# Optimization experiments

Measured on AMD Instinct MI355X. Metric: run time of the kernel, lower is better.

## Reference

```python
import jax, jax.numpy as jnp
import numpy as np

IN_CAPS = 1152
OUT_CAPS = 10
IN_DIM = 8
OUT_DIM = 16
ROUTING_ITERS = 3
BATCH = 512


def squash(s, axis=-1, eps=1e-8):
    # v = (||s||^2 / (1 + ||s||^2)) * s / ||s||
    mag_sq = jnp.sum(s * s, axis=axis, keepdims=True)
    mag = jnp.sqrt(mag_sq + eps)
    return (mag_sq / (1.0 + mag_sq)) * (s / mag)


def setup_inputs() -> dict:
    key = jax.random.key(0)
    kx, kw = jax.random.split(key)
    x = jax.random.normal(kx, (BATCH, IN_CAPS, IN_DIM), dtype=jnp.float32)
    stdv = 1.0 / np.sqrt(IN_CAPS)
    W = jax.random.uniform(kw, (IN_CAPS, OUT_CAPS, OUT_DIM, IN_DIM),
                           minval=-stdv, maxval=stdv, dtype=jnp.float32)
    return {"x": x, "W": W}


def reference(x, W):
    # u_hat[b,i,j,:] = W[i,j] @ x[b,i]  -> [B, 1152, 10, 16]
    u_hat = jnp.einsum('ijde,bie->bijd', W, x)
    u_det = jax.lax.stop_gradient(u_hat)
    b = jnp.zeros((x.shape[0], IN_CAPS, OUT_CAPS), dtype=x.dtype)
    v = None
    for it in range(ROUTING_ITERS):
        c = jax.nn.softmax(b, axis=2)  # softmax over out capsules
        u = u_hat if it == ROUTING_ITERS - 1 else u_det
        s = jnp.einsum('bij,bijd->bjd', c, u)  # [B, 10, 16]
        v = squash(s, axis=-1)
        if it != ROUTING_ITERS - 1:
            # agreement: u_hat . v  -> [B, 1152, 10]
            b = b + jnp.einsum('bijd,bjd->bij', u_det, v)
    return v  # [B, 10, 16]
```

## Files before the change

### kernel.cpp

```cpp
#include <hip/hip_runtime.h>
#include <math.h>

#define J 10
#define BT 16
#define NBT 32
#define NIC 16
#define ICB 72
#define IPW 18
#define JD 160
#define BATCH 512
#define IN_CAPS 1152
#define RTH 256

typedef __attribute__((ext_vector_type(8))) short short8;
typedef __attribute__((ext_vector_type(4))) float f32x4;

__device__ inline short f2bf(float f) {
    union { float f; unsigned u; } v; v.f = f;
    return (short)((v.u + 0x7FFFu + ((v.u >> 16) & 1u)) >> 16);
}
__device__ inline short8 cvt8(float4 a, float4 b) {
    short8 o;
    o[0] = f2bf(a.x); o[1] = f2bf(a.y); o[2] = f2bf(a.z); o[3] = f2bf(a.w);
    o[4] = f2bf(b.x); o[5] = f2bf(b.y); o[6] = f2bf(b.z); o[7] = f2bf(b.w);
    return o;
}

__global__ __launch_bounds__(256) void convert_w(
    const float* __restrict__ W, short* __restrict__ Wb, short* __restrict__ zb)
{
    const int t = blockIdx.x * 256 + threadIdx.x;
    const float4* src = (const float4*)W + (size_t)t * 2;
    *(short8*)(Wb + (size_t)t * 8) = cvt8(src[0], src[1]);
    if (blockIdx.x == 0 && threadIdx.x < 32) zb[threadIdx.x] = 0;
}

#define TI 32
#define TB 64
__global__ __launch_bounds__(256) void transpose_x(
    const float* __restrict__ X, short* __restrict__ Xb)
{
    __shared__ short8 tile[TI][TB + 1];
    const int it = blockIdx.x % (IN_CAPS / TI);
    const int bt = blockIdx.x / (IN_CAPS / TI);
    const int t  = threadIdx.x;

    const int i_l = t & 31, b_s = t >> 5;
#pragma unroll
    for (int p = 0; p < 8; ++p) {
        const int b_l = p * 8 + b_s;
        const float4* src = (const float4*)(X +
            (((size_t)(bt * TB + b_l)) * IN_CAPS + it * TI + i_l) * 8);
        tile[i_l][b_l] = cvt8(src[0], src[1]);
    }
    __syncthreads();
    const int b_l = t & 63, i_s = t >> 6;
#pragma unroll
    for (int p = 0; p < 8; ++p) {
        const int i_l2 = p * 4 + i_s;
        *(short8*)(Xb + (((size_t)(it * TI + i_l2)) * BATCH + bt * TB + b_l) * 8)
            = tile[i_l2][b_l];
    }
}

template<int MODE>
__global__ __launch_bounds__(RTH, 2) void route_kernel(
    const short* __restrict__ Xb, const short* __restrict__ Wb,
    const short* __restrict__ zb, const float* __restrict__ V,
    float* __restrict__ S_part)
{
    __shared__ float s_lds[BT][JD + 1];
    const int tid   = threadIdx.x;
    const int lane  = tid & 63, wave = tid >> 6;
    const int icb   = blockIdx.x % NIC;
    const int btile = blockIdx.x / NIC;
    const int bcol  = lane & 15, kg = lane >> 4;
    const int b     = btile * BT + bcol;

    for (int t = tid; t < BT * (JD + 1); t += RTH) (&s_lds[0][0])[t] = 0.f;
    __syncthreads();

    if (MODE == 0) {
        f32x4 acc[J];
#pragma unroll
        for (int j = 0; j < J; ++j) acc[j] = (f32x4)(0.f);
        for (int ks = wave; ks < ICB / 4; ks += 4) {
            const int ia = icb * ICB + ks * 4 + kg;
            const short8 bfr = *(const short8*)(Xb + ((size_t)ia * BATCH + b) * 8);
            short8 afr[J];
#pragma unroll
            for (int j = 0; j < J; ++j)
                afr[j] = *(const short8*)(Wb + (size_t)ia * 1280 + j * 128 + bcol * 8);
#pragma unroll
            for (int j = 0; j < J; ++j)
                acc[j] = __builtin_amdgcn_mfma_f32_16x16x32_bf16(afr[j], bfr, acc[j], 0, 0, 0);
        }
#pragma unroll
        for (int j = 0; j < J; ++j)
#pragma unroll
            for (int r = 0; r < 4; ++r)
                atomicAdd(&s_lds[bcol][j * 16 + kg * 4 + r], 0.1f * acc[j][r]);
    } else {
        float4 Vr[J];
#pragma unroll
        for (int j = 0; j < J; ++j)
            Vr[j] = *(const float4*)(V + (size_t)b * JD + j * 16 + kg * 4);

        float s_acc[J][4];
#pragma unroll
        for (int j = 0; j < J; ++j)
#pragma unroll
            for (int r = 0; r < 4; ++r) s_acc[j][r] = 0.f;

        const bool act = (lane < 16);
        const short* xb0 = act ? (Xb + (size_t)b * 8) : zb;
        const size_t xis = act ? (size_t)BATCH * 8 : 0;
        const short* wb0 = act ? (Wb + (size_t)bcol * 8) : zb;
        const size_t wis = act ? 1280 : 0;
        const int    wjs = act ? 128 : 0;

        const int i0w = icb * ICB + wave * IPW;
        for (int ii = 0; ii < IPW; ++ii) {
            const size_t i = (size_t)(i0w + ii);
            short8 afr[J];
#pragma unroll
            for (int j = 0; j < J; ++j)
                afr[j] = *(const short8*)(wb0 + i * wis + j * wjs);
            const short8 bfr = *(const short8*)(xb0 + i * xis);

            f32x4 u[J];
#pragma unroll
            for (int j = 0; j < J; ++j)
                u[j] = __builtin_amdgcn_mfma_f32_16x16x32_bf16(afr[j], bfr, (f32x4)(0.f), 0, 0, 0);

            float L[J];
#pragma unroll
            for (int j = 0; j < J; ++j)
                L[j] = u[j][0] * Vr[j].x + u[j][1] * Vr[j].y
                     + u[j][2] * Vr[j].z + u[j][3] * Vr[j].w;
#pragma unroll
            for (int j = 0; j < J; ++j) {
                L[j] += __shfl_xor(L[j], 16);
                L[j] += __shfl_xor(L[j], 32);
            }
            float c[J], Z = 0.f;
#pragma unroll
            for (int j = 0; j < J; ++j) { c[j] = __expf(L[j]); Z += c[j]; }
            const float rz = 1.0f / Z;
#pragma unroll
            for (int j = 0; j < J; ++j) {
                const float cj = c[j] * rz;
                s_acc[j][0] += cj * u[j][0];
                s_acc[j][1] += cj * u[j][1];
                s_acc[j][2] += cj * u[j][2];
                s_acc[j][3] += cj * u[j][3];
            }
        }
#pragma unroll
        for (int j = 0; j < J; ++j)
#pragma unroll
            for (int r = 0; r < 4; ++r)
                atomicAdd(&s_lds[bcol][j * 16 + kg * 4 + r], s_acc[j][r]);
    }
    __syncthreads();

    for (int t = tid; t < BT * JD; t += RTH) {
        const int bb = t / JD, p = t % JD;
        S_part[((size_t)icb * BATCH + btile * BT + bb) * JD + p] = s_lds[bb][p];
    }
}

__global__ __launch_bounds__(256) void squash_kernel(
    const float* __restrict__ S_part, float* __restrict__ V,
    float* __restrict__ out, int mode)
{
    const int t = blockIdx.x * 256 + threadIdx.x;
    float s = 0.f;
#pragma unroll
    for (int ic = 0; ic < NIC; ic++)
        s += S_part[(size_t)ic * BATCH * JD + t];
    float sq = s * s;
    sq += __shfl_xor(sq, 1);
    sq += __shfl_xor(sq, 2);
    sq += __shfl_xor(sq, 4);
    sq += __shfl_xor(sq, 8);
    const float v = s * sq / ((1.f + sq) * sqrtf(sq + 1e-8f));
    if (mode == 0)      V[t] = v;
    else if (mode == 1) V[t] += v;
    else                out[t] = v;
}

extern "C" void kernel_launch(void* const* d_in, const int* in_sizes, int n_in,
                              void* d_out, int out_size, void* d_ws, size_t ws_size,
                              hipStream_t stream)
{
    const float* X = (const float*)d_in[0];
    const float* W = (const float*)d_in[1];
    float* out = (float*)d_out;

    float* S_part = (float*)d_ws;
    float* V      = S_part + (size_t)NIC * BATCH * JD;
    short* Wb     = (short*)(V + (size_t)BATCH * JD);
    short* Xb     = Wb + (size_t)IN_CAPS * JD * 8;
    short* zb     = Xb + (size_t)IN_CAPS * BATCH * 8;

    const dim3 rg(NBT * NIC), rb(RTH);
    const dim3 sg(BATCH * JD / 256), sb(256);

    convert_w<<<dim3(720), dim3(256), 0, stream>>>(W, Wb, zb);
    transpose_x<<<dim3((IN_CAPS / TI) * (BATCH / TB)), dim3(256), 0, stream>>>(X, Xb);

    route_kernel<0><<<rg, rb, 0, stream>>>(Xb, Wb, zb, V, S_part);
    squash_kernel<<<sg, sb, 0, stream>>>(S_part, V, out, 0);
    route_kernel<1><<<rg, rb, 0, stream>>>(Xb, Wb, zb, V, S_part);
    squash_kernel<<<sg, sb, 0, stream>>>(S_part, V, out, 1);
    route_kernel<1><<<rg, rb, 0, stream>>>(Xb, Wb, zb, V, S_part);
    squash_kernel<<<sg, sb, 0, stream>>>(S_part, V, out, 2);
}
```

Before: 158.3 us.

## Stage W tiles in LDS and re-split input-capsule partition for routing kernel

The routing kernel now copies each 16-capsule chunk of bf16 W into shared memory, using a padded row stride, and reads MFMA A-fragments from LDS instead of global memory. The input-capsule dimension is re-split into 36 blocks of 32 capsules, processed in two phases, and the occupancy hint rises from 2 to 3 blocks per CU. The aim is to cut redundant global/L2 traffic for W across lanes and waves and to add parallelism. In exchange it adds more S_part partials for squash to reduce, extra barriers, and LDS pressure that may limit occupancy.

```diff
diff --git a/kernel.cpp b/kernel.cpp
--- a/kernel.cpp
+++ b/kernel.cpp
@@ -4,13 +4,15 @@
 #define J 10
 #define BT 16
 #define NBT 32
-#define NIC 16
-#define ICB 72
-#define IPW 18
+#define NIC 36
+#define ICB 32
+#define ICH 16
 #define JD 160
 #define BATCH 512
 #define IN_CAPS 1152
 #define RTH 256
+#define WSS 1296
+#define ZOFF (ICH * WSS)
 
 typedef __attribute__((ext_vector_type(8))) short short8;
 typedef __attribute__((ext_vector_type(4))) float f32x4;
@@ -64,11 +66,12 @@
 }
 
 template<int MODE>
-__global__ __launch_bounds__(RTH, 2) void route_kernel(
+__global__ __launch_bounds__(RTH, 3) void route_kernel(
     const short* __restrict__ Xb, const short* __restrict__ Wb,
     const short* __restrict__ zb, const float* __restrict__ V,
     float* __restrict__ S_part)
 {
+    __shared__ __align__(16) short Ws[ICH * WSS + 32];
     __shared__ float s_lds[BT][JD + 1];
     const int tid   = threadIdx.x;
     const int lane  = tid & 63, wave = tid >> 6;
@@ -78,84 +81,101 @@
     const int b     = btile * BT + bcol;
 
     for (int t = tid; t < BT * (JD + 1); t += RTH) (&s_lds[0][0])[t] = 0.f;
-    __syncthreads();
-
+    if (tid < 32) Ws[ZOFF + tid] = 0;
+
+    f32x4 acc[J];
+    float4 Vr[J];
+    float s_acc[J][4];
     if (MODE == 0) {
-        f32x4 acc[J];
 #pragma unroll
         for (int j = 0; j < J; ++j) acc[j] = (f32x4)(0.f);
-        for (int ks = wave; ks < ICB / 4; ks += 4) {
-            const int ia = icb * ICB + ks * 4 + kg;
-            const short8 bfr = *(const short8*)(Xb + ((size_t)ia * BATCH + b) * 8);
+    } else {
+#pragma unroll
+        for (int j = 0; j < J; ++j) {
+            Vr[j] = *(const float4*)(V + (size_t)b * JD + j * 16 + kg * 4);
+#pragma unroll
+            for (int r = 0; r < 4; ++r) s_acc[j][r] = 0.f;
+        }
+    }
+
+    const bool act = (lane < 16);
+    const short* xb0 = act ? (Xb + (size_t)b * 8) : zb;
+    const size_t xis = act ? (size_t)BATCH * 8 : 0;
+    const int joff = act ? 128 : 0;
+
+    for (int ph = 0; ph < 2; ++ph) {
+        __syncthreads();
+        {
+            const short8* src = (const short8*)(Wb + ((size_t)(icb * ICB + ph * ICH)) * 1280);
+            for (int t = tid; t < ICH * 160; t += RTH) {
+                const int iloc = t / 160, r = t - iloc * 160;
+                *(short8*)&Ws[iloc * WSS + r * 8] = src[t];
+            }
+        }
+        __syncthreads();
+
+        if (MODE == 0) {
+            const int iloc = wave * 4 + kg;
+            const int ig   = icb * ICB + ph * ICH + iloc;
+            const short8 bfr = *(const short8*)(Xb + ((size_t)ig * BATCH + b) * 8);
             short8 afr[J];
 #pragma unroll
             for (int j = 0; j < J; ++j)
-                afr[j] = *(const short8*)(Wb + (size_t)ia * 1280 + j * 128 + bcol * 8);
+                afr[j] = *(const short8*)&Ws[iloc * WSS + j * 128 + bcol * 8];
 #pragma unroll
             for (int j = 0; j < J; ++j)
                 acc[j] = __builtin_amdgcn_mfma_f32_16x16x32_bf16(afr[j], bfr, acc[j], 0, 0, 0);
+        } else {
+            const int i0 = icb * ICB + ph * ICH + wave * 4;
+            short8 bx[4];
+#pragma unroll
+            for (int t2 = 0; t2 < 4; ++t2)
+                bx[t2] = *(const short8*)(xb0 + (size_t)(i0 + t2) * xis);
+
+#pragma unroll 2
+            for (int ii = 0; ii < 4; ++ii) {
+                const int iloc = wave * 4 + ii;
+                const int abase = act ? (iloc * WSS + bcol * 8) : ZOFF;
+                f32x4 u[J];
+#pragma unroll
+                for (int j = 0; j < J; ++j) {
+                    const short8 afr = *(const short8*)&Ws[abase + j * joff];
+                    u[j] = __builtin_amdgcn_mfma_f32_16x16x32_bf16(afr, bx[ii], (f32x4)(0.f), 0, 0, 0);
+                }
+                float L[J];
+#pragma unroll
+                for (int j = 0; j < J; ++j)
+                    L[j] = u[j][0] * Vr[j].x + u[j][1] * Vr[j].y
+                         + u[j][2] * Vr[j].z + u[j][3] * Vr[j].w;
+#pragma unroll
+                for (int j = 0; j < J; ++j) {
+                    L[j] += __shfl_xor(L[j], 16);
+                    L[j] += __shfl_xor(L[j], 32);
+                }
+                float c[J], Z = 0.f;
+#pragma unroll
+                for (int j = 0; j < J; ++j) { c[j] = __expf(L[j]); Z += c[j]; }
+                const float rz = 1.0f / Z;
+#pragma unroll
+                for (int j = 0; j < J; ++j) {
+                    const float cj = c[j] * rz;
+                    s_acc[j][0] += cj * u[j][0];
+                    s_acc[j][1] += cj * u[j][1];
+                    s_acc[j][2] += cj * u[j][2];
+                    s_acc[j][3] += cj * u[j][3];
+                }
+            }
         }
+    }
+
+    __syncthreads();
+    if (MODE == 0) {
 #pragma unroll
         for (int j = 0; j < J; ++j)
 #pragma unroll
             for (int r = 0; r < 4; ++r)
                 atomicAdd(&s_lds[bcol][j * 16 + kg * 4 + r], 0.1f * acc[j][r]);
     } else {
-        float4 Vr[J];
-#pragma unroll
-        for (int j = 0; j < J; ++j)
-            Vr[j] = *(const float4*)(V + (size_t)b * JD + j * 16 + kg * 4);
-
-        float s_acc[J][4];
-#pragma unroll
-        for (int j = 0; j < J; ++j)
-#pragma unroll
-            for (int r = 0; r < 4; ++r) s_acc[j][r] = 0.f;
-
-        const bool act = (lane < 16);
-        const short* xb0 = act ? (Xb + (size_t)b * 8) : zb;
-        const size_t xis = act ? (size_t)BATCH * 8 : 0;
-        const short* wb0 = act ? (Wb + (size_t)bcol * 8) : zb;
-        const size_t wis = act ? 1280 : 0;
-        const int    wjs = act ? 128 : 0;
-
-        const int i0w = icb * ICB + wave * IPW;
-        for (int ii = 0; ii < IPW; ++ii) {
-            const size_t i = (size_t)(i0w + ii);
-            short8 afr[J];
-#pragma unroll
-            for (int j = 0; j < J; ++j)
-                afr[j] = *(const short8*)(wb0 + i * wis + j * wjs);
-            const short8 bfr = *(const short8*)(xb0 + i * xis);
-
-            f32x4 u[J];
-#pragma unroll
-            for (int j = 0; j < J; ++j)
-                u[j] = __builtin_amdgcn_mfma_f32_16x16x32_bf16(afr[j], bfr, (f32x4)(0.f), 0, 0, 0);
-
-            float L[J];
-#pragma unroll
-            for (int j = 0; j < J; ++j)
-                L[j] = u[j][0] * Vr[j].x + u[j][1] * Vr[j].y
-                     + u[j][2] * Vr[j].z + u[j][3] * Vr[j].w;
-#pragma unroll
-            for (int j = 0; j < J; ++j) {
-                L[j] += __shfl_xor(L[j], 16);
-                L[j] += __shfl_xor(L[j], 32);
-            }
-            float c[J], Z = 0.f;
-#pragma unroll
-            for (int j = 0; j < J; ++j) { c[j] = __expf(L[j]); Z += c[j]; }
-            const float rz = 1.0f / Z;
-#pragma unroll
-            for (int j = 0; j < J; ++j) {
-                const float cj = c[j] * rz;
-                s_acc[j][0] += cj * u[j][0];
-                s_acc[j][1] += cj * u[j][1];
-                s_acc[j][2] += cj * u[j][2];
-                s_acc[j][3] += cj * u[j][3];
-            }
-        }
 #pragma unroll
         for (int j = 0; j < J; ++j)
 #pragma unroll
```

Result: slower. 422.4 us (+166.8%).
